# Kernel optimization log

Hardware: AMD Instinct MI355X
Metric: run time of the kernel (lower is better)

## Reference

```python
import jax, jax.numpy as jnp
import numpy as np

D_MODEL = 1024
N_HEADS = 16
N_PHASE = 128              # 8 * n_heads
PHASE_PER_HEAD = N_PHASE // N_HEADS   # 8
HEAD_DIM = D_MODEL // N_HEADS         # 64
B, L = 2, 2048
SCALE = 1.0 / np.sqrt(PHASE_PER_HEAD)
LN_EPS = 1e-5


def _pos_phase(seq_len, n_phase, base=10000.0):
    # RoPE-style frequencies; even and odd columns both carry sinusoid
    inv_freq = 1.0 / base ** (jnp.arange(0, n_phase, 2, dtype=jnp.float32) / n_phase)
    sinusoid = jnp.arange(seq_len, dtype=jnp.float32)[:, None] * inv_freq[None, :]  # (L, n_phase//2)
    return jnp.repeat(sinusoid, 2, axis=1)  # (L, n_phase): cols 0::2 and 1::2 equal sinusoid


def setup_inputs() -> dict:
    key = jax.random.key(0)
    ks = jax.random.split(key, 10)
    xavier = lambda k, shp: jax.random.normal(k, shp, jnp.float32) * np.sqrt(2.0 / (shp[0] + shp[1]))
    return {
        "x_real": jax.random.normal(ks[0], (B, L, D_MODEL), jnp.float32),
        "x_imag": jax.random.normal(ks[1], (B, L, D_MODEL), jnp.float32),
        "Wq": xavier(ks[2], (N_PHASE, D_MODEL)),
        "bq": jax.random.uniform(ks[3], (N_PHASE,), jnp.float32, -np.pi, np.pi),
        "Wk": xavier(ks[4], (N_PHASE, D_MODEL)),
        "bk": jax.random.uniform(ks[5], (N_PHASE,), jnp.float32, -np.pi, np.pi),
        "Wv": xavier(ks[6], (D_MODEL, D_MODEL)),
        "Wo": xavier(ks[7], (D_MODEL, D_MODEL)) / np.sqrt(2.0),
        "gamma": jnp.ones((D_MODEL,), jnp.float32),
        "beta": jnp.zeros((D_MODEL,), jnp.float32),
    }


def reference(x_real, x_imag, Wq, bq, Wk, bk, Wv, Wo, gamma, beta):
    b, l, d = x_real.shape
    pos = _pos_phase(l, N_PHASE)  # (L, n_phase), constant buffer

    # additive phase with position injection
    Qt = (x_imag @ Wq.T + bq + pos).reshape(b, l, N_HEADS, PHASE_PER_HEAD).transpose(0, 2, 1, 3)
    Kt = (x_imag @ Wk.T + bk + pos).reshape(b, l, N_HEADS, PHASE_PER_HEAD).transpose(0, 2, 1, 3)

    # cos(Qi)cos(Kj) + sin(Qi)sin(Kj) as one contraction over stacked features
    qf = jnp.concatenate([jnp.cos(Qt), jnp.sin(Qt)], axis=-1)  # (B,H,L,2P)
    kf = jnp.concatenate([jnp.cos(Kt), jnp.sin(Kt)], axis=-1)
    scores = jnp.einsum('bhip,bhjp->bhij', qf, kf) * SCALE     # (B,H,L,L)

    causal = jnp.triu(jnp.ones((l, l), dtype=bool), 1)
    scores = jnp.where(causal, -jnp.inf, scores)
    attn = jax.nn.softmax(scores, axis=-1)

    V = (x_real @ Wv.T).reshape(b, l, N_HEADS, HEAD_DIM).transpose(0, 2, 1, 3)  # (B,H,L,hd)
    out = jnp.einsum('bhij,bhjd->bhid', attn, V)
    out = out.transpose(0, 2, 1, 3).reshape(b, l, d) @ Wo.T

    # residual + LayerNorm (eps matches torch default)
    h = x_real + out
    mu = jnp.mean(h, axis=-1, keepdims=True)
    var = jnp.mean(jnp.square(h - mu), axis=-1, keepdims=True)
    out_real = (h - mu) * jax.lax.rsqrt(var + LN_EPS) * gamma + beta
    return (out_real, x_imag)
```

## Files before the change

kernel.cpp:

```cpp
#include <hip/hip_runtime.h>
#include <math.h>

#define D_MODEL 1024
#define N_HEADS 16
#define N_PHASE 128
#define HEAD_DIM 64
#define B_SZ 2
#define L_SEQ 2048
#define QK_SCALE 0.35355339059327373f
#define LN_EPS 1e-5f
#define POS_COEF 0.07195578415606394f
#define INV_2PI 0.15915494309189535f

typedef __attribute__((ext_vector_type(8))) short bf16x8;
typedef __attribute__((ext_vector_type(4))) short s16x4;
typedef __attribute__((ext_vector_type(4))) float f32x4;

__device__ __forceinline__ float wave_reduce_sum(float v) {
#pragma unroll
  for (int off = 32; off > 0; off >>= 1) v += __shfl_xor(v, off);
  return v;
}
__device__ __forceinline__ unsigned short f2bf(float x) {
  unsigned u = __float_as_uint(x);
  u += 0x7fffu + ((u >> 16) & 1u);
  return (unsigned short)(u >> 16);
}
__device__ __forceinline__ void gload16(const short* g, short* l) {
  __builtin_amdgcn_global_load_lds(
      (const __attribute__((address_space(1))) void*)g,
      (__attribute__((address_space(3))) void*)l, 16, 0, 0);
}
__device__ __forceinline__ void fast_sincos(float ang, float* s, float* c) {
  float rev = ang * INV_2PI;
  rev = rev - rintf(rev);
  *c = __builtin_amdgcn_cosf(rev);
  *s = __builtin_amdgcn_sinf(rev);
}

#define NX4 ((B_SZ * L_SEQ * D_MODEL) / 4)
#define NWP4 ((N_PHASE * D_MODEL) / 4)
#define NW4 ((D_MODEL * D_MODEL) / 4)
__device__ __forceinline__ s16x4 cvt4(float4 v) {
  s16x4 o;
  o[0] = (short)f2bf(v.x);
  o[1] = (short)f2bf(v.y);
  o[2] = (short)f2bf(v.z);
  o[3] = (short)f2bf(v.w);
  return o;
}
__global__ __launch_bounds__(256) void cvtall_kernel(
    const float* __restrict__ x_real, const float* __restrict__ x_imag,
    const float* __restrict__ Wq, const float* __restrict__ Wk,
    const float* __restrict__ Wv, const float* __restrict__ Wo,
    short* __restrict__ xr_bf, short* __restrict__ xi_bf,
    short* __restrict__ Wq_bf, short* __restrict__ Wk_bf,
    short* __restrict__ Wv_bf, short* __restrict__ Wo_bf,
    float* __restrict__ outi) {
  const int i = blockIdx.x * 256 + threadIdx.x;
  if (i < NX4) {
    const float4 vi = ((const float4*)x_imag)[i];
    ((float4*)outi)[i] = vi;
    ((s16x4*)xi_bf)[i] = cvt4(vi);
    ((s16x4*)xr_bf)[i] = cvt4(((const float4*)x_real)[i]);
  } else if (i < NX4 + NWP4) {
    const int j = i - NX4;
    ((s16x4*)Wq_bf)[j] = cvt4(((const float4*)Wq)[j]);
    ((s16x4*)Wk_bf)[j] = cvt4(((const float4*)Wk)[j]);
  } else if (i < NX4 + NWP4 + NW4) {
    const int j = i - NX4 - NWP4;
    ((s16x4*)Wv_bf)[j] = cvt4(((const float4*)Wv)[j]);
    ((s16x4*)Wo_bf)[j] = cvt4(((const float4*)Wo)[j]);
  }
}

__device__ __forceinline__ void gemm_core(const short* __restrict__ A,
                                          const short* __restrict__ Bm, int K,
                                          int mBase, int nBase,
                                          f32x4 acc[4][2], short* As,
                                          short* Bs) {
  const int tid = threadIdx.x;
  const int wv = tid >> 6, ln = tid & 63;
  const int wr = wv >> 1, wc = wv & 1;
  const int fr = ln & 15, fc = ln >> 4;
  const int row8 = ln >> 3;
  const int cg = (ln & 7) ^ row8;
  const short* ga = A + (size_t)(mBase + wv * 32 + row8) * K + cg * 8;
  const short* gb = Bm + (size_t)(nBase + wv * 16 + row8) * K + cg * 8;
  short* la = As + wv * 2048;
  short* lb = Bs + wv * 1024;
  const int swz = fr & 7;

  for (int k0 = 0; k0 < K; k0 += 64) {
    __syncthreads();
#pragma unroll
    for (int i = 0; i < 4; ++i)
      gload16(ga + k0 + (size_t)(8 * i) * K, la + i * 512);
#pragma unroll
    for (int i = 0; i < 2; ++i)
      gload16(gb + k0 + (size_t)(8 * i) * K, lb + i * 512);
    __syncthreads();

    bf16x8 af[2][4], bfr[2][2];
#pragma unroll
    for (int kk = 0; kk < 2; ++kk) {
      const int pc = ((kk * 4 + fc) ^ swz) * 8;
#pragma unroll
      for (int mi = 0; mi < 4; ++mi)
        af[kk][mi] =
            *(const bf16x8*)&As[(wr * 64 + mi * 16 + fr) * 64 + pc];
#pragma unroll
      for (int ni = 0; ni < 2; ++ni)
        bfr[kk][ni] =
            *(const bf16x8*)&Bs[(wc * 32 + ni * 16 + fr) * 64 + pc];
    }
#pragma unroll
    for (int kk = 0; kk < 2; ++kk)
#pragma unroll
      for (int mi = 0; mi < 4; ++mi)
#pragma unroll
        for (int ni = 0; ni < 2; ++ni)
          acc[mi][ni] = __builtin_amdgcn_mfma_f32_16x16x32_bf16(
              af[kk][mi], bfr[kk][ni], acc[mi][ni], 0, 0, 0);
  }
}

__global__ __launch_bounds__(256) void qkv_kernel(
    const short* __restrict__ xi, const short* __restrict__ xr,
    const short* __restrict__ WqB, const short* __restrict__ WkB,
    const short* __restrict__ WvB, const float* __restrict__ bq,
    const float* __restrict__ bk, short* __restrict__ qf,
    short* __restrict__ kf, short* __restrict__ Vt) {
  __shared__ short As[128 * 64];
  __shared__ short Bs[64 * 64];
  const int y = blockIdx.y;
  const int mBase = blockIdx.x * 128;
  const short* A;
  const short* Bm;
  int nBase;
  if (y < 4) {
    A = xi;
    Bm = (y < 2) ? WqB : WkB;
    nBase = (y & 1) * 64;
  } else {
    A = xr;
    Bm = WvB;
    nBase = (y - 4) * 64;
  }

  f32x4 acc[4][2];
#pragma unroll
  for (int i = 0; i < 4; ++i)
#pragma unroll
    for (int j = 0; j < 2; ++j) acc[i][j] = (f32x4){0.f, 0.f, 0.f, 0.f};
  gemm_core(A, Bm, D_MODEL, mBase, nBase, acc, As, Bs);

  const int ln = threadIdx.x & 63, wv = threadIdx.x >> 6;
  const int wr = wv >> 1, wc = wv & 1;
  const int fr = ln & 15, fc = ln >> 4;

  if (y < 4) {
    const float* bias = (y < 2) ? bq : bk;
    short* Cs = (y < 2) ? qf : kf;
    const float fscale = (y < 2) ? QK_SCALE : 1.0f;
#pragma unroll
    for (int mi = 0; mi < 4; ++mi)
#pragma unroll
      for (int ni = 0; ni < 2; ++ni)
#pragma unroll
        for (int r = 0; r < 4; ++r) {
          const int m = mBase + wr * 64 + mi * 16 + fc * 4 + r;
          const int n = nBase + wc * 32 + ni * 16 + fr;
          const int b = m >> 11, l = m & (L_SEQ - 1);
          const float inv_freq = __expf(-(float)(n & ~1) * POS_COEF);
          const float ang = acc[mi][ni][r] + bias[n] + (float)l * inv_freq;
          float sv, cv;
          fast_sincos(ang, &sv, &cv);
          const int h = n >> 3, p = n & 7;
          const size_t base = ((size_t)((b << 4) + h) * L_SEQ + l) * 16;
          Cs[base + p] = (short)f2bf(cv * fscale);
          Cs[base + 8 + p] = (short)f2bf(sv * fscale);
        }
  } else {
#pragma unroll
    for (int mi = 0; mi < 4; ++mi)
#pragma unroll
      for (int ni = 0; ni < 2; ++ni) {
        const int n = nBase + wc * 32 + ni * 16 + fr;
        const int m = mBase + wr * 64 + mi * 16 + fc * 4;
        const int b = m >> 11, l = m & (L_SEQ - 1);
        const int t = (l >> 2) & 7;
        const int tp = ((t << 1) & 6) | (t >> 2);
        const int lpos = (l & ~31) | (tp << 2);
        const int h = n >> 6, d = n & 63;
        const int jc = lpos >> 5, jlo = lpos & 31;
        const int gg = jlo >> 3, ee = jlo & 7;
        s16x4 pk;
#pragma unroll
        for (int r = 0; r < 4; ++r) pk[r] = (short)f2bf(acc[mi][ni][r]);
        const size_t off = (size_t)((b << 4) + h) * 64 * L_SEQ +
                           (size_t)(jc * 4 + (d >> 4)) * 512 + gg * 128 +
                           (d & 15) * 8 + ee;
        *(s16x4*)&Vt[off] = pk;
      }
  }
}

__global__ __launch_bounds__(256) void ogemm_kernel(
    const short* __restrict__ A, const short* __restrict__ Bm,
    const float* __restrict__ resid, float* __restrict__ Cf) {
  __shared__ short As[128 * 64];
  __shared__ short Bs[64 * 64];
  const int mBase = blockIdx.x * 128, nBase = blockIdx.y * 64;

  f32x4 acc[4][2];
#pragma unroll
  for (int i = 0; i < 4; ++i)
#pragma unroll
    for (int j = 0; j < 2; ++j) acc[i][j] = (f32x4){0.f, 0.f, 0.f, 0.f};
  gemm_core(A, Bm, D_MODEL, mBase, nBase, acc, As, Bs);

  const int ln = threadIdx.x & 63, wv = threadIdx.x >> 6;
  const int wr = wv >> 1, wc = wv & 1;
  const int fr = ln & 15, fc = ln >> 4;
#pragma unroll
  for (int mi = 0; mi < 4; ++mi)
#pragma unroll
    for (int ni = 0; ni < 2; ++ni)
#pragma unroll
      for (int r = 0; r < 4; ++r) {
        const int m = mBase + wr * 64 + mi * 16 + fc * 4 + r;
        const int n = nBase + wc * 32 + ni * 16 + fr;
        const size_t idx = (size_t)m * D_MODEL + n;
        Cf[idx] = acc[mi][ni][r] + resid[idx];
      }
}

__global__ __launch_bounds__(256) void attn_mfma_kernel(
    const short* __restrict__ qf, const short* __restrict__ kf,
    const short* __restrict__ Vt, short* __restrict__ ao) {
  const int bh = blockIdx.x;
  const int qg = 127 - (int)blockIdx.y;
  const int tid = threadIdx.x;
  const int w = tid >> 6;
  const int lane = tid & 63;
  const int g = lane >> 4;
  const int q16 = lane & 15;
  const int qglob = qg * 16 + q16;
  const int ntiles = (qg >> 2) + 1;

  __shared__ float ol[4][16][68];
  __shared__ float ll[4][16];

  const short* qf_h = qf + (size_t)bh * L_SEQ * 16;
  const short* kf_h = kf + (size_t)bh * L_SEQ * 16;
  const short* Vt_h = Vt + (size_t)bh * 64 * L_SEQ;
  const int b = bh >> 4, h = bh & 15;

  bf16x8 qfrag = {0, 0, 0, 0, 0, 0, 0, 0};
  if (g < 2) qfrag = *(const bf16x8*)(qf_h + (size_t)qglob * 16 + g * 8);

  f32x4 o[4];
#pragma unroll
  for (int dc = 0; dc < 4; ++dc) o[dc] = (f32x4){0.f, 0.f, 0.f, 0.f};
  float lsum = 0.f;

#pragma unroll 1
  for (int t = w; t < ntiles; t += 4) {
    const int j0 = t << 6;

    bf16x8 vf0[4], vf1[4];
#pragma unroll
    for (int dc = 0; dc < 4; ++dc)
      vf0[dc] = *(const bf16x8*)(Vt_h + ((size_t)((2 * t) * 4 + dc) << 9) +
                                 lane * 8);

    bf16x8 kfr[4];
#pragma unroll
    for (int jt = 0; jt < 4; ++jt) {
      kfr[jt] = (bf16x8){0, 0, 0, 0, 0, 0, 0, 0};
      if (g < 2)
        kfr[jt] =
            *(const bf16x8*)(kf_h + (size_t)(j0 + jt * 16 + q16) * 16 + g * 8);
    }

    f32x4 s[4];
#pragma unroll
    for (int jt = 0; jt < 4; ++jt)
      s[jt] = __builtin_amdgcn_mfma_f32_16x16x32_bf16(
          kfr[jt], qfrag, (f32x4){0.f, 0.f, 0.f, 0.f}, 0, 0, 0);

#pragma unroll
    for (int dc = 0; dc < 4; ++dc)
      vf1[dc] = *(const bf16x8*)(Vt_h + ((size_t)((2 * t + 1) * 4 + dc) << 9) +
                                 lane * 8);

    if (t == ntiles - 1) {
#pragma unroll
      for (int jt = 0; jt < 4; ++jt)
#pragma unroll
        for (int r = 0; r < 4; ++r)
          if (j0 + jt * 16 + g * 4 + r > qglob) s[jt][r] = -INFINITY;
    }

    float ex[4][4];
#pragma unroll
    for (int jt = 0; jt < 4; ++jt)
#pragma unroll
      for (int r = 0; r < 4; ++r) {
        ex[jt][r] = __expf(s[jt][r]);
        lsum += ex[jt][r];
      }

#pragma unroll
    for (int c = 0; c < 2; ++c) {
      union {
        unsigned u[4];
        bf16x8 v;
      } pb;
#pragma unroll
      for (int hw = 0; hw < 2; ++hw) {
        asm("v_cvt_pk_bf16_f32 %0, %1, %2"
            : "=v"(pb.u[hw * 2 + 0])
            : "v"(ex[2 * c + hw][0]), "v"(ex[2 * c + hw][1]));
        asm("v_cvt_pk_bf16_f32 %0, %1, %2"
            : "=v"(pb.u[hw * 2 + 1])
            : "v"(ex[2 * c + hw][2]), "v"(ex[2 * c + hw][3]));
      }
      const bf16x8* vfc = c ? vf1 : vf0;
#pragma unroll
      for (int dc = 0; dc < 4; ++dc)
        o[dc] = __builtin_amdgcn_mfma_f32_16x16x32_bf16(vfc[dc], pb.v, o[dc],
                                                        0, 0, 0);
    }
  }

  lsum += __shfl_xor(lsum, 16);
  lsum += __shfl_xor(lsum, 32);
  if (g == 0) ll[w][q16] = lsum;
#pragma unroll
  for (int dc = 0; dc < 4; ++dc)
    *(f32x4*)&ol[w][q16][dc * 16 + g * 4] = o[dc];
  __syncthreads();

  const float lt = (ll[0][q16] + ll[1][q16]) + (ll[2][q16] + ll[3][q16]);
  const float inv = 1.f / lt;
  const int d0 = w * 16 + g * 4;
  s16x4 pk;
#pragma unroll
  for (int r = 0; r < 4; ++r) {
    const float v = ((ol[0][q16][d0 + r] + ol[1][q16][d0 + r]) +
                     (ol[2][q16][d0 + r] + ol[3][q16][d0 + r]));
    pk[r] = (short)f2bf(v * inv);
  }
  short* orow = ao + ((size_t)(b * L_SEQ + qglob)) * D_MODEL + h * 64;
  *(s16x4*)&orow[d0] = pk;
}

__global__ __launch_bounds__(256) void ln_kernel(float* __restrict__ io,
                                                 const float* __restrict__ gamma,
                                                 const float* __restrict__ beta) {
  const int row = blockIdx.x;
  float* p = io + (size_t)row * D_MODEL;
  const int tid = threadIdx.x;
  float4 x = ((const float4*)p)[tid];
  float s = x.x + x.y + x.z + x.w;
  float sq = x.x * x.x + x.y * x.y + x.z * x.z + x.w * x.w;
  s = wave_reduce_sum(s);
  sq = wave_reduce_sum(sq);
  __shared__ float ss[4], ssq[4];
  const int w = tid >> 6, lane = tid & 63;
  if (lane == 0) {
    ss[w] = s;
    ssq[w] = sq;
  }
  __syncthreads();
  s = ss[0] + ss[1] + ss[2] + ss[3];
  sq = ssq[0] + ssq[1] + ssq[2] + ssq[3];
  const float mean = s * (1.f / D_MODEL);
  const float var = sq * (1.f / D_MODEL) - mean * mean;
  const float rstd = rsqrtf(var + LN_EPS);
  const float4 g = ((const float4*)gamma)[tid];
  const float4 bt = ((const float4*)beta)[tid];
  float4 y;
  y.x = (x.x - mean) * rstd * g.x + bt.x;
  y.y = (x.y - mean) * rstd * g.y + bt.y;
  y.z = (x.z - mean) * rstd * g.z + bt.z;
  y.w = (x.w - mean) * rstd * g.w + bt.w;
  ((float4*)p)[tid] = y;
}

extern "C" void kernel_launch(void* const* d_in, const int* in_sizes, int n_in,
                              void* d_out, int out_size, void* d_ws,
                              size_t ws_size, hipStream_t stream) {
  const float* x_real = (const float*)d_in[0];
  const float* x_imag = (const float*)d_in[1];
  const float* Wq = (const float*)d_in[2];
  const float* bq = (const float*)d_in[3];
  const float* Wk = (const float*)d_in[4];
  const float* bk = (const float*)d_in[5];
  const float* Wv = (const float*)d_in[6];
  const float* Wo = (const float*)d_in[7];
  const float* gamma = (const float*)d_in[8];
  const float* beta = (const float*)d_in[9];

  const size_t n_x = (size_t)B_SZ * L_SEQ * D_MODEL;
  const size_t n_w = (size_t)D_MODEL * D_MODEL;
  const size_t n_wp = (size_t)N_PHASE * D_MODEL;
  const size_t n_qf = (size_t)B_SZ * N_HEADS * L_SEQ * 16;

  short* xi_bf = (short*)d_ws;
  short* xr_bf = xi_bf + n_x;
  short* Wq_bf = xr_bf + n_x;
  short* Wk_bf = Wq_bf + n_wp;
  short* Wv_bf = Wk_bf + n_wp;
  short* Wo_bf = Wv_bf + n_w;
  short* qf = Wo_bf + n_w;
  short* kf = qf + n_qf;
  short* Vt = kf + n_qf;
  short* ao_bf = xr_bf;

  float* outr = (float*)d_out;
  float* outi = outr + n_x;

  const dim3 blk(256);
  const int M = B_SZ * L_SEQ;

  const int cvt_blocks = (NX4 + NWP4 + NW4 + 255) / 256;
  cvtall_kernel<<<dim3(cvt_blocks), blk, 0, stream>>>(
      x_real, x_imag, Wq, Wk, Wv, Wo, xr_bf, xi_bf, Wq_bf, Wk_bf, Wv_bf,
      Wo_bf, outi);

  qkv_kernel<<<dim3(M / 128, 20), blk, 0, stream>>>(
      xi_bf, xr_bf, Wq_bf, Wk_bf, Wv_bf, bq, bk, qf, kf, Vt);
  attn_mfma_kernel<<<dim3(B_SZ * N_HEADS, 128), blk, 0, stream>>>(qf, kf, Vt,
                                                                  ao_bf);
  ogemm_kernel<<<dim3(M / 128, D_MODEL / 64), blk, 0, stream>>>(
      ao_bf, Wo_bf, x_real, outr);
  ln_kernel<<<dim3(M), blk, 0, stream>>>(outr, gamma, beta);
}
```

Before: 91.72 us.

## Pair causal query groups per block to balance load and reuse K/V tiles

Each attention block now handles two 16-row query groups, qg and 127-qg, so every block does roughly the same amount of causal work. The K and V fragments loaded for a tile serve both groups, which cuts global loads per query. The grid shrinks from 128 to 64 blocks along y. In exchange each thread holds more registers for two sets of accumulators, there are fewer blocks to schedule, and the epilogue adds an extra shared-memory reduction pass with another barrier.

```diff
diff --git a/kernel.cpp b/kernel.cpp
--- a/kernel.cpp
+++ b/kernel.cpp
@@ -240,14 +240,17 @@
     const short* __restrict__ qf, const short* __restrict__ kf,
     const short* __restrict__ Vt, short* __restrict__ ao) {
   const int bh = blockIdx.x;
-  const int qg = 127 - (int)blockIdx.y;
+  const int qgA = (int)blockIdx.y;
+  const int qgB = 127 - (int)blockIdx.y;
   const int tid = threadIdx.x;
   const int w = tid >> 6;
   const int lane = tid & 63;
   const int g = lane >> 4;
   const int q16 = lane & 15;
-  const int qglob = qg * 16 + q16;
-  const int ntiles = (qg >> 2) + 1;
+  const int qglobA = qgA * 16 + q16;
+  const int qglobB = qgB * 16 + q16;
+  const int ntilesA = (qgA >> 2) + 1;
+  const int ntilesB = (qgB >> 2) + 1;
 
   __shared__ float ol[4][16][68];
   __shared__ float ll[4][16];
@@ -257,16 +260,23 @@
   const short* Vt_h = Vt + (size_t)bh * 64 * L_SEQ;
   const int b = bh >> 4, h = bh & 15;
 
-  bf16x8 qfrag = {0, 0, 0, 0, 0, 0, 0, 0};
-  if (g < 2) qfrag = *(const bf16x8*)(qf_h + (size_t)qglob * 16 + g * 8);
-
-  f32x4 o[4];
-#pragma unroll
-  for (int dc = 0; dc < 4; ++dc) o[dc] = (f32x4){0.f, 0.f, 0.f, 0.f};
-  float lsum = 0.f;
+  bf16x8 qfragA = {0, 0, 0, 0, 0, 0, 0, 0};
+  bf16x8 qfragB = {0, 0, 0, 0, 0, 0, 0, 0};
+  if (g < 2) {
+    qfragA = *(const bf16x8*)(qf_h + (size_t)qglobA * 16 + g * 8);
+    qfragB = *(const bf16x8*)(qf_h + (size_t)qglobB * 16 + g * 8);
+  }
+
+  f32x4 oA[4], oB[4];
+#pragma unroll
+  for (int dc = 0; dc < 4; ++dc) {
+    oA[dc] = (f32x4){0.f, 0.f, 0.f, 0.f};
+    oB[dc] = (f32x4){0.f, 0.f, 0.f, 0.f};
+  }
+  float lsumA = 0.f, lsumB = 0.f;
 
 #pragma unroll 1
-  for (int t = w; t < ntiles; t += 4) {
+  for (int t = w; t < ntilesB; t += 4) {
     const int j0 = t << 6;
 
     bf16x8 vf0[4], vf1[4];
@@ -284,77 +294,144 @@
             *(const bf16x8*)(kf_h + (size_t)(j0 + jt * 16 + q16) * 16 + g * 8);
     }
 
-    f32x4 s[4];
-#pragma unroll
-    for (int jt = 0; jt < 4; ++jt)
-      s[jt] = __builtin_amdgcn_mfma_f32_16x16x32_bf16(
-          kfr[jt], qfrag, (f32x4){0.f, 0.f, 0.f, 0.f}, 0, 0, 0);
-
 #pragma unroll
     for (int dc = 0; dc < 4; ++dc)
       vf1[dc] = *(const bf16x8*)(Vt_h + ((size_t)((2 * t + 1) * 4 + dc) << 9) +
                                  lane * 8);
 
-    if (t == ntiles - 1) {
+    {
+      f32x4 s[4];
 #pragma unroll
       for (int jt = 0; jt < 4; ++jt)
-#pragma unroll
-        for (int r = 0; r < 4; ++r)
-          if (j0 + jt * 16 + g * 4 + r > qglob) s[jt][r] = -INFINITY;
+        s[jt] = __builtin_amdgcn_mfma_f32_16x16x32_bf16(
+            kfr[jt], qfragB, (f32x4){0.f, 0.f, 0.f, 0.f}, 0, 0, 0);
+      if (t == ntilesB - 1) {
+#pragma unroll
+        for (int jt = 0; jt < 4; ++jt)
+#pragma unroll
+          for (int r = 0; r < 4; ++r)
+            if (j0 + jt * 16 + g * 4 + r > qglobB) s[jt][r] = -INFINITY;
+      }
+      float ex[4][4];
+#pragma unroll
+      for (int jt = 0; jt < 4; ++jt)
+#pragma unroll
+        for (int r = 0; r < 4; ++r) {
+          ex[jt][r] = __expf(s[jt][r]);
+          lsumB += ex[jt][r];
+        }
+#pragma unroll
+      for (int c = 0; c < 2; ++c) {
+        union {
+          unsigned u[4];
+          bf16x8 v;
+        } pb;
+#pragma unroll
+        for (int hw = 0; hw < 2; ++hw) {
+          asm("v_cvt_pk_bf16_f32 %0, %1, %2"
+              : "=v"(pb.u[hw * 2 + 0])
+              : "v"(ex[2 * c + hw][0]), "v"(ex[2 * c + hw][1]));
+          asm("v_cvt_pk_bf16_f32 %0, %1, %2"
+              : "=v"(pb.u[hw * 2 + 1])
+              : "v"(ex[2 * c + hw][2]), "v"(ex[2 * c + hw][3]));
+        }
+        const bf16x8* vfc = c ? vf1 : vf0;
+#pragma unroll
+        for (int dc = 0; dc < 4; ++dc)
+          oB[dc] = __builtin_amdgcn_mfma_f32_16x16x32_bf16(vfc[dc], pb.v,
+                                                           oB[dc], 0, 0, 0);
+      }
     }
 
-    float ex[4][4];
-#pragma unroll
-    for (int jt = 0; jt < 4; ++jt)
-#pragma unroll
-      for (int r = 0; r < 4; ++r) {
-        ex[jt][r] = __expf(s[jt][r]);
-        lsum += ex[jt][r];
+    if (t < ntilesA) {
+      f32x4 s[4];
+#pragma unroll
+      for (int jt = 0; jt < 4; ++jt)
+        s[jt] = __builtin_amdgcn_mfma_f32_16x16x32_bf16(
+            kfr[jt], qfragA, (f32x4){0.f, 0.f, 0.f, 0.f}, 0, 0, 0);
+      if (t == ntilesA - 1) {
+#pragma unroll
+        for (int jt = 0; jt < 4; ++jt)
+#pragma unroll
+          for (int r = 0; r < 4; ++r)
+            if (j0 + jt * 16 + g * 4 + r > qglobA) s[jt][r] = -INFINITY;
       }
-
-#pragma unroll
-    for (int c = 0; c < 2; ++c) {
-      union {
-        unsigned u[4];
-        bf16x8 v;
-      } pb;
-#pragma unroll
-      for (int hw = 0; hw < 2; ++hw) {
-        asm("v_cvt_pk_bf16_f32 %0, %1, %2"
-            : "=v"(pb.u[hw * 2 + 0])
-            : "v"(ex[2 * c + hw][0]), "v"(ex[2 * c + hw][1]));
-        asm("v_cvt_pk_bf16_f32 %0, %1, %2"
-            : "=v"(pb.u[hw * 2 + 1])
-            : "v"(ex[2 * c + hw][2]), "v"(ex[2 * c + hw][3]));
+      float ex[4][4];
+#pragma unroll
+      for (int jt = 0; jt < 4; ++jt)
+#pragma unroll
+        for (int r = 0; r < 4; ++r) {
+          ex[jt][r] = __expf(s[jt][r]);
+          lsumA += ex[jt][r];
+        }
+#pragma unroll
+      for (int c = 0; c < 2; ++c) {
+        union {
+          unsigned u[4];
+          bf16x8 v;
+        } pb;
+#pragma unroll
+        for (int hw = 0; hw < 2; ++hw) {
+          asm("v_cvt_pk_bf16_f32 %0, %1, %2"
+              : "=v"(pb.u[hw * 2 + 0])
+              : "v"(ex[2 * c + hw][0]), "v"(ex[2 * c + hw][1]));
+          asm("v_cvt_pk_bf16_f32 %0, %1, %2"
+              : "=v"(pb.u[hw * 2 + 1])
+              : "v"(ex[2 * c + hw][2]), "v"(ex[2 * c + hw][3]));
+        }
+        const bf16x8* vfc = c ? vf1 : vf0;
+#pragma unroll
+        for (int dc = 0; dc < 4; ++dc)
+          oA[dc] = __builtin_amdgcn_mfma_f32_16x16x32_bf16(vfc[dc], pb.v,
+                                                           oA[dc], 0, 0, 0);
       }
-      const bf16x8* vfc = c ? vf1 : vf0;
-#pragma unroll
-      for (int dc = 0; dc < 4; ++dc)
-        o[dc] = __builtin_amdgcn_mfma_f32_16x16x32_bf16(vfc[dc], pb.v, o[dc],
-                                                        0, 0, 0);
     }
   }
 
-  lsum += __shfl_xor(lsum, 16);
-  lsum += __shfl_xor(lsum, 32);
-  if (g == 0) ll[w][q16] = lsum;
+  lsumB += __shfl_xor(lsumB, 16);
+  lsumB += __shfl_xor(lsumB, 32);
+  if (g == 0) ll[w][q16] = lsumB;
 #pragma unroll
   for (int dc = 0; dc < 4; ++dc)
-    *(f32x4*)&ol[w][q16][dc * 16 + g * 4] = o[dc];
+    *(f32x4*)&ol[w][q16][dc * 16 + g * 4] = oB[dc];
   __syncthreads();
-
-  const float lt = (ll[0][q16] + ll[1][q16]) + (ll[2][q16] + ll[3][q16]);
-  const float inv = 1.f / lt;
-  const int d0 = w * 16 + g * 4;
-  s16x4 pk;
-#pragma unroll
-  for (int r = 0; r < 4; ++r) {
-    const float v = ((ol[0][q16][d0 + r] + ol[1][q16][d0 + r]) +
-                     (ol[2][q16][d0 + r] + ol[3][q16][d0 + r]));
-    pk[r] = (short)f2bf(v * inv);
-  }
-  short* orow = ao + ((size_t)(b * L_SEQ + qglob)) * D_MODEL + h * 64;
-  *(s16x4*)&orow[d0] = pk;
+  {
+    const float lt = (ll[0][q16] + ll[1][q16]) + (ll[2][q16] + ll[3][q16]);
+    const float inv = 1.f / lt;
+    const int d0 = w * 16 + g * 4;
+    s16x4 pk;
+#pragma unroll
+    for (int r = 0; r < 4; ++r) {
+      const float v = ((ol[0][q16][d0 + r] + ol[1][q16][d0 + r]) +
+                       (ol[2][q16][d0 + r] + ol[3][q16][d0 + r]));
+      pk[r] = (short)f2bf(v * inv);
+    }
+    short* orow = ao + ((size_t)(b * L_SEQ + qglobB)) * D_MODEL + h * 64;
+    *(s16x4*)&orow[d0] = pk;
+  }
+  __syncthreads();
+
+  lsumA += __shfl_xor(lsumA, 16);
+  lsumA += __shfl_xor(lsumA, 32);
+  if (g == 0) ll[w][q16] = lsumA;
+#pragma unroll
+  for (int dc = 0; dc < 4; ++dc)
+    *(f32x4*)&ol[w][q16][dc * 16 + g * 4] = oA[dc];
+  __syncthreads();
+  {
+    const float lt = (ll[0][q16] + ll[1][q16]) + (ll[2][q16] + ll[3][q16]);
+    const float inv = 1.f / lt;
+    const int d0 = w * 16 + g * 4;
+    s16x4 pk;
+#pragma unroll
+    for (int r = 0; r < 4; ++r) {
+      const float v = ((ol[0][q16][d0 + r] + ol[1][q16][d0 + r]) +
+                       (ol[2][q16][d0 + r] + ol[3][q16][d0 + r]));
+      pk[r] = (short)f2bf(v * inv);
+    }
+    short* orow = ao + ((size_t)(b * L_SEQ + qglobA)) * D_MODEL + h * 64;
+    *(s16x4*)&orow[d0] = pk;
+  }
 }
 
 __global__ __launch_bounds__(256) void ln_kernel(float* __restrict__ io,
@@ -433,8 +510,8 @@
 
   qkv_kernel<<<dim3(M / 128, 20), blk, 0, stream>>>(
       xi_bf, xr_bf, Wq_bf, Wk_bf, Wv_bf, bq, bk, qf, kf, Vt);
-  attn_mfma_kernel<<<dim3(B_SZ * N_HEADS, 128), blk, 0, stream>>>(qf, kf, Vt,
-                                                                  ao_bf);
+  attn_mfma_kernel<<<dim3(B_SZ * N_HEADS, 64), blk, 0, stream>>>(qf, kf, Vt,
+                                                                 ao_bf);
   ogemm_kernel<<<dim3(M / 128, D_MODEL / 64), blk, 0, stream>>>(
       ao_bf, Wo_bf, x_real, outr);
   ln_kernel<<<dim3(M), blk, 0, stream>>>(outr, gamma, beta);
```

Result: no change. 89.98 us (-1.9%).
